# Optimization experiments

Measured on AMD Instinct MI355X. Metric: run time of the kernel, lower is better.

Reference implementation:

```python
import jax, jax.numpy as jnp
import numpy as np

WINDOW = 5
MAX_LEVELS = 4
EPS = 1e-6

_SX = (jnp.array([[-1., 0., 1.], [-2., 0., 2.], [-1., 0., 1.]], dtype=jnp.float32) / 8.0).reshape(1, 1, 3, 3)
_SY = jnp.transpose(_SX, (0, 1, 3, 2))
_DN = ('NCHW', 'OIHW', 'NCHW')


def _avg_pool2(x):
    B, C, H, W = x.shape
    return x.reshape(B, C, H // 2, 2, W // 2, 2).mean(axis=(3, 5))


def _warp(img, flow):
    # bilinear grid_sample, align_corners=True, zeros padding; sample at pixel coords grid+flow
    B, C, H, W = img.shape
    ys, xs = jnp.meshgrid(jnp.arange(H, dtype=img.dtype), jnp.arange(W, dtype=img.dtype), indexing='ij')
    x = xs[None] + flow[:, 0]  # [B,H,W]
    y = ys[None] + flow[:, 1]
    x0f, y0f = jnp.floor(x), jnp.floor(y)
    wx, wy = x - x0f, y - y0f
    imf = img.reshape(B, C, H * W)

    def gather(yi, xi):
        valid = (xi >= 0) & (xi <= W - 1) & (yi >= 0) & (yi <= H - 1)
        xi_c = jnp.clip(xi, 0, W - 1).astype(jnp.int32)
        yi_c = jnp.clip(yi, 0, H - 1).astype(jnp.int32)
        flat = (yi_c * W + xi_c).reshape(B, 1, H * W)
        v = jnp.take_along_axis(imf, jnp.broadcast_to(flat, (B, C, H * W)), axis=2).reshape(B, C, H, W)
        return v * valid[:, None].astype(img.dtype)

    out = (gather(y0f, x0f) * ((1 - wx) * (1 - wy))[:, None]
           + gather(y0f, x0f + 1) * (wx * (1 - wy))[:, None]
           + gather(y0f + 1, x0f) * ((1 - wx) * wy)[:, None]
           + gather(y0f + 1, x0f + 1) * (wx * wy)[:, None])
    return out


def _resize_ac(x, Hn, Wn):
    # bilinear resize, align_corners=True (static shapes)
    B, C, H, W = x.shape
    if (H, W) == (Hn, Wn):
        return x
    ys = jnp.linspace(0.0, H - 1, Hn, dtype=x.dtype)
    xs = jnp.linspace(0.0, W - 1, Wn, dtype=x.dtype)
    y0 = jnp.clip(jnp.floor(ys), 0, H - 2).astype(jnp.int32)
    x0 = jnp.clip(jnp.floor(xs), 0, W - 2).astype(jnp.int32)
    wy = (ys - y0)[None, None, :, None]
    wx = (xs - x0)[None, None, None, :]
    rows = x[:, :, y0, :] * (1 - wy) + x[:, :, y0 + 1, :] * wy
    return rows[:, :, :, x0] * (1 - wx) + rows[:, :, :, x0 + 1] * wx


def _lucas_kanade(I1, I2):
    if I1.shape[1] > 1:
        I1 = I1.mean(1, keepdims=True)
        I2 = I2.mean(1, keepdims=True)
    Ix = jax.lax.conv_general_dilated(I1, _SX, (1, 1), [(1, 1), (1, 1)], dimension_numbers=_DN)
    Iy = jax.lax.conv_general_dilated(I1, _SY, (1, 1), [(1, 1), (1, 1)], dimension_numbers=_DN)
    It = I2 - I1
    # stack all 5 structure-tensor products and box-filter them with one grouped conv
    stats = jnp.concatenate([Ix * Ix, Iy * Iy, Ix * Iy, Ix * It, Iy * It], axis=1)  # [B,5,H,W]
    boxk = jnp.ones((5, 1, WINDOW, WINDOW), dtype=I1.dtype)
    p0 = WINDOW // 2
    p1 = WINDOW - p0 - 1
    S = jax.lax.conv_general_dilated(stats, boxk, (1, 1), [(p0, p1), (p0, p1)],
                                     feature_group_count=5, dimension_numbers=_DN)
    Sxx, Syy, Sxy, Sxt, Syt = jnp.split(S, 5, axis=1)
    inv = 1.0 / (Sxx * Syy - Sxy * Sxy + EPS)
    u = (-Syy * Sxt + Sxy * Syt) * inv
    v = (Sxy * Sxt - Sxx * Syt) * inv
    return jnp.concatenate([u, v], axis=1)


def setup_inputs() -> dict:
    key = jax.random.key(0)
    k1, k2 = jax.random.split(key)
    img1 = jax.random.uniform(k1, (8, 3, 512, 512), dtype=jnp.float32)
    img2 = jax.random.uniform(k2, (8, 3, 512, 512), dtype=jnp.float32)
    return {"img1": img1, "img2": img2}


def reference(img1, img2):
    B, C, H, W = img1.shape
    levels = max(1, MAX_LEVELS)
    pyr1, pyr2 = [img1], [img2]
    for _ in range(1, levels):
        pyr1.append(_avg_pool2(pyr1[-1]))
        pyr2.append(_avg_pool2(pyr2[-1]))
    flow = jnp.zeros((B, 2, pyr1[-1].shape[2], pyr1[-1].shape[3]), dtype=img1.dtype)
    for lvl in range(levels - 1, -1, -1):
        I1, I2 = pyr1[lvl], pyr2[lvl]
        if lvl < levels - 1:
            flow = _resize_ac(flow, I1.shape[2], I1.shape[3]) * 2.0
        I2w = _warp(I2, flow)
        flow = flow + _lucas_kanade(I1, I2w)
    if flow.shape[2:] != (H, W):
        fh, fw = flow.shape[2], flow.shape[3]
        flow = _resize_ac(flow, H, W)
        flow = flow * jnp.array([W / fw, H / fh], dtype=flow.dtype).reshape(1, 2, 1, 1)
    return flow
```

## Files before the change

### kernel.cpp

```cpp
#include <hip/hip_runtime.h>

#define NB 8

typedef float f2 __attribute__((ext_vector_type(2)));

__global__ void gray_pool_kernel(const float* __restrict__ img1, const float* __restrict__ img2,
                                 float* __restrict__ g0a, float* __restrict__ g0b,
                                 float* __restrict__ g1a, float* __restrict__ g1b) {
    const int W = 512, HW = 512 * 512, Wq = 256, HWq = 256 * 256;
    int i = blockIdx.x * blockDim.x + threadIdx.x;
    if (i >= NB * HWq) return;
    int qx = i % Wq;
    int qy = (i / Wq) % Wq;
    int b = i / HWq;
    size_t base = (size_t)b * 3 * HW + (size_t)(2 * qy) * W + 2 * qx;
    const float third = 1.0f / 3.0f;

    f2 a0c0 = __builtin_nontemporal_load((const f2*)(img1 + base));
    f2 a1c0 = __builtin_nontemporal_load((const f2*)(img1 + base + W));
    f2 a0c1 = __builtin_nontemporal_load((const f2*)(img1 + base + HW));
    f2 a1c1 = __builtin_nontemporal_load((const f2*)(img1 + base + HW + W));
    f2 a0c2 = __builtin_nontemporal_load((const f2*)(img1 + base + 2 * HW));
    f2 a1c2 = __builtin_nontemporal_load((const f2*)(img1 + base + 2 * HW + W));
    float p00 = (a0c0.x + a0c1.x + a0c2.x) * third;
    float p01 = (a0c0.y + a0c1.y + a0c2.y) * third;
    float p10 = (a1c0.x + a1c1.x + a1c2.x) * third;
    float p11 = (a1c0.y + a1c1.y + a1c2.y) * third;
    size_t gbase = (size_t)b * HW + (size_t)(2 * qy) * W + 2 * qx;
    *(f2*)(g0a + gbase) = (f2){p00, p01};
    *(f2*)(g0a + gbase + W) = (f2){p10, p11};
    g1a[(size_t)b * HWq + qy * Wq + qx] = (p00 + p01 + p10 + p11) * 0.25f;

    f2 b0c0 = __builtin_nontemporal_load((const f2*)(img2 + base));
    f2 b1c0 = __builtin_nontemporal_load((const f2*)(img2 + base + W));
    f2 b0c1 = __builtin_nontemporal_load((const f2*)(img2 + base + HW));
    f2 b1c1 = __builtin_nontemporal_load((const f2*)(img2 + base + HW + W));
    f2 b0c2 = __builtin_nontemporal_load((const f2*)(img2 + base + 2 * HW));
    f2 b1c2 = __builtin_nontemporal_load((const f2*)(img2 + base + 2 * HW + W));
    float q00 = (b0c0.x + b0c1.x + b0c2.x) * third;
    float q01 = (b0c0.y + b0c1.y + b0c2.y) * third;
    float q10 = (b1c0.x + b1c1.x + b1c2.x) * third;
    float q11 = (b1c0.y + b1c1.y + b1c2.y) * third;
    *(f2*)(g0b + gbase) = (f2){q00, q01};
    *(f2*)(g0b + gbase + W) = (f2){q10, q11};
    g1b[(size_t)b * HWq + qy * Wq + qx] = (q00 + q01 + q10 + q11) * 0.25f;
}

__global__ void down2_kernel(const float* __restrict__ l1a, const float* __restrict__ l1b,
                             float* __restrict__ l2a, float* __restrict__ l2b,
                             float* __restrict__ l3a, float* __restrict__ l3b) {
    const int W3 = 64, W2 = 128, W1 = 256;
    int i = blockIdx.x * blockDim.x + threadIdx.x;
    int total = 2 * NB * W3 * W3;
    if (i >= total) return;
    int x3 = i % W3;
    int y3 = (i / W3) % W3;
    int b = (i / (W3 * W3)) % NB;
    int j = i / (NB * W3 * W3);
    const float* l1 = (j ? l1b : l1a) + (size_t)b * W1 * W1;
    float* l2 = (j ? l2b : l2a) + (size_t)b * W2 * W2;
    float* l3 = (j ? l3b : l3a) + (size_t)b * W3 * W3;
    float4 r0 = *(const float4*)(l1 + (size_t)(4 * y3 + 0) * W1 + 4 * x3);
    float4 r1 = *(const float4*)(l1 + (size_t)(4 * y3 + 1) * W1 + 4 * x3);
    float4 r2 = *(const float4*)(l1 + (size_t)(4 * y3 + 2) * W1 + 4 * x3);
    float4 r3 = *(const float4*)(l1 + (size_t)(4 * y3 + 3) * W1 + 4 * x3);
    float a00 = (r0.x + r0.y + r1.x + r1.y) * 0.25f;
    float a01 = (r0.z + r0.w + r1.z + r1.w) * 0.25f;
    float a10 = (r2.x + r2.y + r3.x + r3.y) * 0.25f;
    float a11 = (r2.z + r2.w + r3.z + r3.w) * 0.25f;
    *(f2*)(l2 + (size_t)(2 * y3) * W2 + 2 * x3) = (f2){a00, a01};
    *(f2*)(l2 + (size_t)(2 * y3 + 1) * W2 + 2 * x3) = (f2){a10, a11};
    l3[y3 * W3 + x3] = (a00 + a01 + a10 + a11) * 0.25f;
}

template <int MODE, int H, int W, int TH>
__global__ __launch_bounds__(256, 4) void lk_roll(
    const float* __restrict__ g1, const float* __restrict__ g2,
    const float* __restrict__ fin, float* __restrict__ fout) {
    constexpr int XT = (W + 57) / 58;
    constexpr int YT = H / TH;
    constexpr int TILES = XT * YT;
    constexpr int Hs = H / 2, Ws = W / 2;
    constexpr float scale = (float)(Hs - 1) / (float)(H - 1);

    const int lane = threadIdx.x & 63;
    const int wid = threadIdx.x >> 6;
    const int b = blockIdx.x % NB;
    const int tix = (blockIdx.x / NB) * 4 + wid;
    if (tix >= TILES) return;
    const int xt = tix % XT, yt = tix / XT;
    const int x = xt * 58 - 3 + lane;
    const bool xin = (x >= 0) && (x < W);

    const float* G1 = g1 + (size_t)b * H * W;
    const float* G2 = g2 + (size_t)b * H * W;
    float* FO = fout + (size_t)b * 2 * H * W;

    const int p0 = yt * TH - 2;

    int cx0 = 0;
    float wxf = 0.0f;
    const float* FU = nullptr;
    const float* FV = nullptr;
    int y0cur = 0;
    float u00 = 0.f, u01 = 0.f, u10 = 0.f, u11 = 0.f;
    float v00 = 0.f, v01 = 0.f, v10 = 0.f, v11 = 0.f;
    if (MODE) {
        FU = fin + (size_t)b * 2 * Hs * Ws;
        FV = FU + Hs * Ws;
        float sx = (float)x * scale;
        cx0 = min(max((int)sx, 0), Ws - 2);
        wxf = sx - (float)cx0;
        y0cur = min(max((int)((float)p0 * scale), 0), Hs - 2);
        const float* pu = FU + y0cur * Ws + cx0;
        const float* pv = FV + y0cur * Ws + cx0;
        u00 = pu[0]; u01 = pu[1]; u10 = pu[Ws]; u11 = pu[Ws + 1];
        v00 = pv[0]; v01 = pv[1]; v10 = pv[Ws]; v11 = pv[Ws + 1];
    }

    auto issue = [&](int yy) -> float {
        return (xin && yy >= 0 && yy < H) ? G1[yy * W + x] : 0.0f;
    };
    auto dands = [&](float gv, float& d, float& s) {
        float gl = __shfl_up(gv, 1);
        float gr = __shfl_down(gv, 1);
        d = gr - gl;
        s = gl + 2.0f * gv + gr;
    };
    auto hs5 = [&](float v) {
        float a = __shfl_down(v, 1);
        float c = __shfl_down(v, 2);
        float t = v + a + c;
        return __shfl_up(t, 2) + a + c;
    };

    float hxx[5], hyy[5], hxy[5], hxt[5], hyt[5];
#pragma unroll
    for (int k = 0; k < 5; ++k) { hxx[k] = hyy[k] = hxy[k] = hxt[k] = hyt[k] = 0.0f; }
    float su1 = 0.f, su2 = 0.f, sv1 = 0.f, sv2 = 0.f;

    float dm, d0, sm, s0, dp, sp;
    float gA = issue(p0 - 1);
    float gc = issue(p0);
    dands(gA, dm, sm);
    dands(gc, d0, s0);

#pragma unroll
    for (int i = 0; i < TH + 4; ++i) {
        const int yc = p0 + i;
        float gn = issue(yc + 1);

        float su = 0.0f, sv = 0.0f;
        if (MODE) {
            int y0i = min(max((int)((float)yc * scale), 0), Hs - 2);
            if (y0i != y0cur) {
                u00 = u10; u01 = u11; v00 = v10; v01 = v11;
                const float* pu = FU + (y0i + 1) * Ws + cx0;
                const float* pv = FV + (y0i + 1) * Ws + cx0;
                u10 = pu[0]; u11 = pu[1];
                v10 = pv[0]; v11 = pv[1];
                y0cur = y0i;
            }
            float wyf = (float)yc * scale - (float)y0cur;
            float ut = u00 + (u10 - u00) * wyf;
            float ub = u01 + (u11 - u01) * wyf;
            float vt = v00 + (v10 - v00) * wyf;
            float vb = v01 + (v11 - v01) * wyf;
            su = 2.0f * (ut + (ub - ut) * wxf);
            sv = 2.0f * (vt + (vb - vt) * wxf);
        }

        float I2w;
        if (MODE) {
            float xx = (float)x + su, yy2 = (float)yc + sv;
            float x0f = floorf(xx), y0f = floorf(yy2);
            float wx = xx - x0f, wy = yy2 - y0f;
            int xi = (int)x0f, yi = (int)y0f;
            int xa = min(max(xi, 0), W - 1), xb = min(max(xi + 1, 0), W - 1);
            int ya = min(max(yi, 0), H - 1), yb = min(max(yi + 1, 0), H - 1);
            float w00 = G2[ya * W + xa];
            float w01 = G2[ya * W + xb];
            float w10 = G2[yb * W + xa];
            float w11 = G2[yb * W + xb];
            float mx0 = (xi >= 0 && xi < W) ? 1.0f : 0.0f;
            float mx1 = (xi >= -1 && xi < W - 1) ? 1.0f : 0.0f;
            float my0 = (yi >= 0 && yi < H) ? 1.0f : 0.0f;
            float my1 = (yi >= -1 && yi < H - 1) ? 1.0f : 0.0f;
            I2w = w00 * ((1.0f - wx) * (1.0f - wy) * mx0 * my0)
                + w01 * (wx * (1.0f - wy) * mx1 * my0)
                + w10 * ((1.0f - wx) * wy * mx0 * my1)
                + w11 * (wx * wy * mx1 * my1);
        } else {
            I2w = (xin && yc >= 0 && yc < H) ? G2[yc * W + x] : 0.0f;
        }

        dands(gn, dp, sp);
        float Ix = (dm + 2.0f * d0 + dp) * 0.125f;
        float Iy = (sp - sm) * 0.125f;
        float It = I2w - gc;
        float vm = (xin && yc >= 0 && yc < H) ? 1.0f : 0.0f;
        Ix *= vm; Iy *= vm; It *= vm;

        const int k = i % 5;
        hxx[k] = Ix * Ix;
        hyy[k] = Iy * Iy;
        hxy[k] = Ix * Iy;
        hxt[k] = Ix * It;
        hyt[k] = Iy * It;

        if (i >= 4) {
            float vxx = hxx[0] + hxx[1] + hxx[2] + hxx[3] + hxx[4];
            float vyy = hyy[0] + hyy[1] + hyy[2] + hyy[3] + hyy[4];
            float vxy = hxy[0] + hxy[1] + hxy[2] + hxy[3] + hxy[4];
            float vxt = hxt[0] + hxt[1] + hxt[2] + hxt[3] + hxt[4];
            float vyt = hyt[0] + hyt[1] + hyt[2] + hyt[3] + hyt[4];
            float Sxx = hs5(vxx);
            float Syy = hs5(vyy);
            float Sxy = hs5(vxy);
            float Sxt = hs5(vxt);
            float Syt = hs5(vyt);
            float inv = 1.0f / (Sxx * Syy - Sxy * Sxy + 1e-6f);
            float du = (-Syy * Sxt + Sxy * Syt) * inv;
            float dv = (Sxy * Sxt - Sxx * Syt) * inv;
            int yo = yc - 2;
            if (lane >= 3 && lane <= 60 && x < W) {
                FO[yo * W + x] = su2 + du;
                FO[H * W + yo * W + x] = sv2 + dv;
            }
        }
        su2 = su1; su1 = su;
        sv2 = sv1; sv1 = sv;
        dm = d0; d0 = dp;
        sm = s0; s0 = sp;
        gc = gn;
    }
}

extern "C" void kernel_launch(void* const* d_in, const int* in_sizes, int n_in,
                              void* d_out, int out_size, void* d_ws, size_t ws_size,
                              hipStream_t stream) {
    const float* img1 = (const float*)d_in[0];
    const float* img2 = (const float*)d_in[1];
    float* out = (float*)d_out;
    float* ws = (float*)d_ws;

    const int Hl[4] = {512, 256, 128, 64};
    size_t goff[4];
    size_t tot = 0;
    for (int l = 0; l < 4; ++l) {
        goff[l] = tot;
        tot += (size_t)NB * Hl[l] * Hl[l];
    }
    float* p1 = ws;
    float* p2 = ws + tot;
    float* f64 = p2 + tot;
    float* f128 = f64 + (size_t)NB * 2 * 64 * 64;
    float* f256 = f128 + (size_t)NB * 2 * 128 * 128;

    {
        int n = NB * 256 * 256;
        gray_pool_kernel<<<(n + 255) / 256, 256, 0, stream>>>(
            img1, img2, p1 + goff[0], p2 + goff[0], p1 + goff[1], p2 + goff[1]);
    }
    {
        int n = 2 * NB * 64 * 64;
        down2_kernel<<<(n + 255) / 256, 256, 0, stream>>>(
            p1 + goff[1], p2 + goff[1], p1 + goff[2], p2 + goff[2], p1 + goff[3], p2 + goff[3]);
    }
    {
        const int tiles = 2 * 16;
        lk_roll<0, 64, 64, 4><<<NB * ((tiles + 3) / 4), 256, 0, stream>>>(
            p1 + goff[3], p2 + goff[3], nullptr, f64);
    }
    {
        const int tiles = 3 * 32;
        lk_roll<1, 128, 128, 4><<<NB * ((tiles + 3) / 4), 256, 0, stream>>>(
            p1 + goff[2], p2 + goff[2], f64, f128);
    }
    {
        const int tiles = 5 * 64;
        lk_roll<1, 256, 256, 4><<<NB * ((tiles + 3) / 4), 256, 0, stream>>>(
            p1 + goff[1], p2 + goff[1], f128, f256);
    }
    {
        const int tiles = 9 * 128;
        lk_roll<1, 512, 512, 4><<<NB * ((tiles + 3) / 4), 256, 0, stream>>>(
            p1 + goff[0], p2 + goff[0], f256, out);
    }
}
```

Baseline: 66.86 us.

## Batch all row loads and warp gathers ahead of the LK compute loop

Restructures the rolling Lucas-Kanade kernel so that all G1 rows, the G2 rows (or the upsampled flow and the four bilinear warp-gather samples) for the whole tile column are loaded into register arrays before the compute loop runs. This exposes many independent global loads at once so their latency overlaps, instead of each iteration waiting on its own loads. In exchange, register pressure rises considerably with TH, which risks spills or lower occupancy under the 256x4 launch bounds.

After: 65.19 us. -2.5%, faster.

```diff
diff --git a/kernel.cpp b/kernel.cpp
--- a/kernel.cpp
+++ b/kernel.cpp
@@ -80,6 +80,7 @@
     constexpr int XT = (W + 57) / 58;
     constexpr int YT = H / TH;
     constexpr int TILES = XT * YT;
+    constexpr int NR = TH + 4;
     constexpr int Hs = H / 2, Ws = W / 2;
     constexpr float scale = (float)(Hs - 1) / (float)(H - 1);
 
@@ -98,27 +99,7 @@
 
     const int p0 = yt * TH - 2;
 
-    int cx0 = 0;
-    float wxf = 0.0f;
-    const float* FU = nullptr;
-    const float* FV = nullptr;
-    int y0cur = 0;
-    float u00 = 0.f, u01 = 0.f, u10 = 0.f, u11 = 0.f;
-    float v00 = 0.f, v01 = 0.f, v10 = 0.f, v11 = 0.f;
-    if (MODE) {
-        FU = fin + (size_t)b * 2 * Hs * Ws;
-        FV = FU + Hs * Ws;
-        float sx = (float)x * scale;
-        cx0 = min(max((int)sx, 0), Ws - 2);
-        wxf = sx - (float)cx0;
-        y0cur = min(max((int)((float)p0 * scale), 0), Hs - 2);
-        const float* pu = FU + y0cur * Ws + cx0;
-        const float* pv = FV + y0cur * Ws + cx0;
-        u00 = pu[0]; u01 = pu[1]; u10 = pu[Ws]; u11 = pu[Ws + 1];
-        v00 = pv[0]; v01 = pv[1]; v10 = pv[Ws]; v11 = pv[Ws + 1];
-    }
-
-    auto issue = [&](int yy) -> float {
+    auto issue1 = [&](int yy) -> float {
         return (xin && yy >= 0 && yy < H) ? G1[yy * W + x] : 0.0f;
     };
     auto dands = [&](float gv, float& d, float& s) {
@@ -134,31 +115,42 @@
         return __shfl_up(t, 2) + a + c;
     };
 
-    float hxx[5], hyy[5], hxy[5], hxt[5], hyt[5];
-#pragma unroll
-    for (int k = 0; k < 5; ++k) { hxx[k] = hyy[k] = hxy[k] = hxt[k] = hyt[k] = 0.0f; }
-    float su1 = 0.f, su2 = 0.f, sv1 = 0.f, sv2 = 0.f;
-
-    float dm, d0, sm, s0, dp, sp;
-    float gA = issue(p0 - 1);
-    float gc = issue(p0);
-    dands(gA, dm, sm);
-    dands(gc, d0, s0);
-
-#pragma unroll
-    for (int i = 0; i < TH + 4; ++i) {
-        const int yc = p0 + i;
-        float gn = issue(yc + 1);
-
-        float su = 0.0f, sv = 0.0f;
-        if (MODE) {
+    float g[NR + 2];
+#pragma unroll
+    for (int j = 0; j < NR + 2; ++j) g[j] = issue1(p0 - 1 + j);
+
+    float i2d[MODE ? 1 : NR];
+    if (!MODE) {
+#pragma unroll
+        for (int i = 0; i < NR; ++i) {
+            int yc = p0 + i;
+            i2d[i] = (xin && yc >= 0 && yc < H) ? G2[yc * W + x] : 0.0f;
+        }
+    }
+
+    float su[MODE ? NR : 1], sv[MODE ? NR : 1];
+    float w00[MODE ? NR : 1], w01[MODE ? NR : 1], w10[MODE ? NR : 1], w11[MODE ? NR : 1];
+    if (MODE) {
+        const float* FU = fin + (size_t)b * 2 * Hs * Ws;
+        const float* FV = FU + Hs * Ws;
+        float sx = (float)x * scale;
+        int cx0 = min(max((int)sx, 0), Ws - 2);
+        float wxf = sx - (float)cx0;
+        int y0cur = min(max((int)((float)p0 * scale), 0), Hs - 2);
+        const float* pu = FU + y0cur * Ws + cx0;
+        const float* pv = FV + y0cur * Ws + cx0;
+        float u00 = pu[0], u01 = pu[1], u10 = pu[Ws], u11 = pu[Ws + 1];
+        float v00 = pv[0], v01 = pv[1], v10 = pv[Ws], v11 = pv[Ws + 1];
+#pragma unroll
+        for (int i = 0; i < NR; ++i) {
+            int yc = p0 + i;
             int y0i = min(max((int)((float)yc * scale), 0), Hs - 2);
             if (y0i != y0cur) {
                 u00 = u10; u01 = u11; v00 = v10; v01 = v11;
-                const float* pu = FU + (y0i + 1) * Ws + cx0;
-                const float* pv = FV + (y0i + 1) * Ws + cx0;
-                u10 = pu[0]; u11 = pu[1];
-                v10 = pv[0]; v11 = pv[1];
+                const float* qu = FU + (y0i + 1) * Ws + cx0;
+                const float* qv = FV + (y0i + 1) * Ws + cx0;
+                u10 = qu[0]; u11 = qu[1];
+                v10 = qv[0]; v11 = qv[1];
                 y0cur = y0i;
             }
             float wyf = (float)yc * scale - (float)y0cur;
@@ -166,38 +158,52 @@
             float ub = u01 + (u11 - u01) * wyf;
             float vt = v00 + (v10 - v00) * wyf;
             float vb = v01 + (v11 - v01) * wyf;
-            su = 2.0f * (ut + (ub - ut) * wxf);
-            sv = 2.0f * (vt + (vb - vt) * wxf);
-        }
+            su[i] = 2.0f * (ut + (ub - ut) * wxf);
+            sv[i] = 2.0f * (vt + (vb - vt) * wxf);
+            float xx = (float)x + su[i], yy2 = (float)yc + sv[i];
+            int xi = (int)floorf(xx), yi = (int)floorf(yy2);
+            int xa = min(max(xi, 0), W - 1), xb = min(max(xi + 1, 0), W - 1);
+            int ya = min(max(yi, 0), H - 1), yb = min(max(yi + 1, 0), H - 1);
+            w00[i] = G2[ya * W + xa];
+            w01[i] = G2[ya * W + xb];
+            w10[i] = G2[yb * W + xa];
+            w11[i] = G2[yb * W + xb];
+        }
+    }
+
+    float hxx[5], hyy[5], hxy[5], hxt[5], hyt[5];
+#pragma unroll
+    for (int k = 0; k < 5; ++k) { hxx[k] = hyy[k] = hxy[k] = hxt[k] = hyt[k] = 0.0f; }
+
+    float dm, d0, sm, s0, dp, sp;
+    dands(g[0], dm, sm);
+    dands(g[1], d0, s0);
+
+#pragma unroll
+    for (int i = 0; i < NR; ++i) {
+        const int yc = p0 + i;
+        dands(g[i + 2], dp, sp);
+        float Ix = (dm + 2.0f * d0 + dp) * 0.125f;
+        float Iy = (sp - sm) * 0.125f;
 
         float I2w;
         if (MODE) {
-            float xx = (float)x + su, yy2 = (float)yc + sv;
+            float xx = (float)x + su[i], yy2 = (float)yc + sv[i];
             float x0f = floorf(xx), y0f = floorf(yy2);
             float wx = xx - x0f, wy = yy2 - y0f;
             int xi = (int)x0f, yi = (int)y0f;
-            int xa = min(max(xi, 0), W - 1), xb = min(max(xi + 1, 0), W - 1);
-            int ya = min(max(yi, 0), H - 1), yb = min(max(yi + 1, 0), H - 1);
-            float w00 = G2[ya * W + xa];
-            float w01 = G2[ya * W + xb];
-            float w10 = G2[yb * W + xa];
-            float w11 = G2[yb * W + xb];
             float mx0 = (xi >= 0 && xi < W) ? 1.0f : 0.0f;
             float mx1 = (xi >= -1 && xi < W - 1) ? 1.0f : 0.0f;
             float my0 = (yi >= 0 && yi < H) ? 1.0f : 0.0f;
             float my1 = (yi >= -1 && yi < H - 1) ? 1.0f : 0.0f;
-            I2w = w00 * ((1.0f - wx) * (1.0f - wy) * mx0 * my0)
-                + w01 * (wx * (1.0f - wy) * mx1 * my0)
-                + w10 * ((1.0f - wx) * wy * mx0 * my1)
-                + w11 * (wx * wy * mx1 * my1);
+            I2w = w00[i] * ((1.0f - wx) * (1.0f - wy) * mx0 * my0)
+                + w01[i] * (wx * (1.0f - wy) * mx1 * my0)
+                + w10[i] * ((1.0f - wx) * wy * mx0 * my1)
+                + w11[i] * (wx * wy * mx1 * my1);
         } else {
-            I2w = (xin && yc >= 0 && yc < H) ? G2[yc * W + x] : 0.0f;
-        }
-
-        dands(gn, dp, sp);
-        float Ix = (dm + 2.0f * d0 + dp) * 0.125f;
-        float Iy = (sp - sm) * 0.125f;
-        float It = I2w - gc;
+            I2w = i2d[i];
+        }
+        float It = I2w - g[i + 1];
         float vm = (xin && yc >= 0 && yc < H) ? 1.0f : 0.0f;
         Ix *= vm; Iy *= vm; It *= vm;
 
@@ -224,15 +230,14 @@
             float dv = (Sxy * Sxt - Sxx * Syt) * inv;
             int yo = yc - 2;
             if (lane >= 3 && lane <= 60 && x < W) {
-                FO[yo * W + x] = su2 + du;
-                FO[H * W + yo * W + x] = sv2 + dv;
+                float ou = du, ov = dv;
+                if (MODE) { ou += su[i - 2]; ov += sv[i - 2]; }
+                FO[yo * W + x] = ou;
+                FO[H * W + yo * W + x] = ov;
             }
         }
-        su2 = su1; su1 = su;
-        sv2 = sv1; sv1 = sv;
         dm = d0; d0 = dp;
         sm = s0; s0 = sp;
-        gc = gn;
     }
 }
 
```
